# Kernel tuning notes

Measured on AMD Instinct MI355X. Metric: run time of the kernel, lower is better.

## Reference

```python
import jax, jax.numpy as jnp
import numpy as np

ALPHA, BETA, LAMB, GAMMA = 1.0, 1.0, 1e-4, 1.0
K_NN, TAU = 50, 0.1
EPS = 1e-8


def _sqdist(A, B):
    # ||a - b||^2, clamped at 0 like the torch code
    d2 = (A * A).sum(1)[:, None] + (B * B).sum(1)[None, :] - 2.0 * (A @ B.T)
    return jnp.maximum(d2, 0.0)


def _mmd(s, t):
    comb = jnp.concatenate([s, t], axis=0)
    sigma_sq = jax.lax.stop_gradient(jnp.median(_sqdist(comb, comb))) / 2.0
    sigma_sq = jnp.where(sigma_sq < 1e-6, jnp.float32(1.0), sigma_sq)
    g = 1.0 / (sigma_sq + EPS)
    kxx = jnp.exp(-g * _sqdist(s, s)).mean()
    kyy = jnp.exp(-g * _sqdist(t, t)).mean()
    kxy = jnp.exp(-g * _sqdist(s, t)).mean()
    return jnp.maximum(kxx + kyy - 2.0 * kxy, 0.0)


def setup_inputs() -> dict:
    key = jax.random.key(0)
    ks = jax.random.split(key, 8)
    B, d, N, Nq, K = 256, 128, 200000, 10000, K_NN
    q_batch = jax.random.normal(ks[0], (B, d), jnp.float32)
    X = jax.random.normal(ks[1], (N, d), jnp.float32)
    W = jax.random.normal(ks[2], (d, d), jnp.float32) * (1.0 / np.sqrt(d))
    b = jnp.zeros((d,), jnp.float32)
    pre_weights = jax.random.uniform(ks[3], (Nq, K), jnp.float32)
    pre_weights = pre_weights / pre_weights.sum(1, keepdims=True)
    pre_indices = jax.random.randint(ks[4], (Nq, K), 0, N)
    q_indices = jax.random.randint(ks[5], (B,), 0, Nq)
    idx = jax.random.randint(ks[6], (B,), 0, N)
    return {"q_batch": q_batch, "X": X, "W": W, "b": b,
            "pre_weights": pre_weights, "pre_indices": pre_indices,
            "q_indices": q_indices, "idx": idx}


def reference(q_batch, X, W, b, pre_weights, pre_indices, q_indices, idx):
    Tq = q_batch @ W.T + b                                   # model(q_batch), Linear(d, d)
    # ---- MMD between mapped queries and a random database batch ----
    loss_dist = _mmd(Tq, X[idx])
    # ---- exact KNN (faiss IndexFlatL2 equivalent) on detached embeddings ----
    d2_all = _sqdist(jax.lax.stop_gradient(Tq), X)           # [B, N]
    _, post_idx = jax.lax.top_k(-d2_all, K_NN)               # [B, K] nearest neighbors
    Xn = X[post_idx]                                         # [B, K, d]
    l2 = ((Tq[:, None, :] - Xn) ** 2).sum(-1)                # [B, K] (grad flows here)
    post_w = jax.nn.softmax(-l2 / TAU, axis=1)
    # ---- union-KL, vectorized over batch (exact torch.unique semantics) ----
    pre_i = pre_indices[q_indices]                           # [B, K]
    pre_w = pre_weights[q_indices]                           # [B, K]
    cat = jnp.concatenate([pre_i, post_idx], axis=1)         # [B, 2K]
    # multiplicity of each id within the concatenated list -> collapse duplicates
    mult = (cat[:, :, None] == cat[:, None, :]).sum(-1).astype(jnp.float32)  # [B, 2K]
    p_raw = jnp.einsum('bmk,bk->bm',
                       (cat[:, :, None] == pre_i[:, None, :]).astype(jnp.float32), pre_w)
    q_raw = jnp.einsum('bmk,bk->bm',
                       (cat[:, :, None] == post_idx[:, None, :]).astype(jnp.float32), post_w)
    p_c = jnp.maximum(p_raw, EPS)
    q_c = jnp.maximum(q_raw, EPS)
    p = p_c / (p_c / mult).sum(1, keepdims=True)             # normalize over union
    q = q_c / (q_c / mult).sum(1, keepdims=True)
    kl = ((p * (jnp.log(p) - jnp.log(q))) / mult).sum(1)     # KL(p || q) per sample
    loss_knn = kl.mean()
    # ---- L2 regularization of model params & anchor loss ----
    loss_reg = 0.5 * ((W ** 2).sum() + (b ** 2).sum())
    loss_anchor = ((Tq - q_batch) ** 2).sum(1).mean()
    total = ALPHA * loss_dist + BETA * loss_knn + LAMB * loss_reg + GAMMA * loss_anchor
    return jnp.stack([total, loss_dist, loss_knn, loss_anchor])
```

## Files before the change

### kernel.cpp

```cpp
#include <hip/hip_runtime.h>
#include <cstdint>

#define D 128
#define NPTS 200000
#define KNN 50
#define CAP 8192
#define NS 8192
#define SLACK 2.0f

#define OFF_ACC    0
#define OFF_SEL    256
#define OFF_CNT    1024
#define OFF_HIST0  17408
#define OFF_HIST12 148480
#define MEMSET_BYTES 214016
#define OFF_COMB   214016
#define OFF_D2     476160
#define OFF_XN     1524736
#define OFF_SAMP   2324736
#define OFF_THR    10713344
#define OFF_CANDI  10714368
#define OFF_KSG    19102976
#define OFF_TQSW   27491584
#define OFF_XBF    27557120

typedef __attribute__((ext_vector_type(8))) short bf16x8;
typedef __attribute__((ext_vector_type(4))) float f32x4;
typedef const __attribute__((address_space(1))) void* gas_p;
typedef __attribute__((address_space(3))) void* las_p;

__device__ __forceinline__ unsigned fkey(float f) {
    unsigned u = __float_as_uint(f);
    return u ^ ((unsigned)((int)u >> 31) | 0x80000000u);
}

__device__ __forceinline__ void stage8k(const unsigned short* __restrict__ g,
                                        unsigned short* l, int w, int lane)
{
    #pragma unroll
    for (int j = 0; j < 2; j++) {
        const unsigned short* gp = g + j * 2048 + w * 512 + lane * 8;
        unsigned short* lp = l + j * 2048 + w * 512;
        __builtin_amdgcn_global_load_lds((gas_p)gp, (las_p)lp, 16, 0, 0);
    }
}

__global__ void k_phase1(const float* __restrict__ q, const float* __restrict__ X,
                         const float* __restrict__ W, const float* __restrict__ bb,
                         const int* __restrict__ idx, float* __restrict__ comb,
                         unsigned short* __restrict__ tqsw, unsigned short* __restrict__ xbf,
                         float* __restrict__ xn, float* __restrict__ acc)
{
    const int blk = blockIdx.x, t = threadIdx.x;
    if (blk < 12500) {
        __shared__ float xr[16];
        const int lr = t & 15;
        if (t < 16) xr[t] = 0.f;
        __syncthreads();
        const float4* src = (const float4*)(X + ((long)(blk * 16 + lr)) * D + (t >> 4) * 8);
        float4 v0 = src[0], v1 = src[1];
        uint4 pk;
        pk.x = (__float_as_uint(v0.x) >> 16) | (__float_as_uint(v0.y) & 0xFFFF0000u);
        pk.y = (__float_as_uint(v0.z) >> 16) | (__float_as_uint(v0.w) & 0xFFFF0000u);
        pk.z = (__float_as_uint(v1.x) >> 16) | (__float_as_uint(v1.y) & 0xFFFF0000u);
        pk.w = (__float_as_uint(v1.z) >> 16) | (__float_as_uint(v1.w) & 0xFFFF0000u);
        *(uint4*)(xbf + (long)blk * 2048 + t * 8) = pk;
        float ssq = v0.x*v0.x + v0.y*v0.y + v0.z*v0.z + v0.w*v0.w
                  + v1.x*v1.x + v1.y*v1.y + v1.z*v1.z + v1.w*v1.w;
        atomicAdd(&xr[lr], ssq);
        __syncthreads();
        if (t < 16) xn[blk * 16 + t] = xr[t];
    } else if (blk < 12628) {
        __shared__ float rowv[2][D];
        __shared__ float red[2][D];
        const int half = t >> 7, tt = t & 127;
        const int row = (blk - 12500) * 2 + half;
        rowv[half][tt] = q[row * D + tt];
        __syncthreads();
        float s = 0.f;
        const float* wr = W + tt * D;
        #pragma unroll 4
        for (int k = 0; k < D; k++) s = fmaf(rowv[half][k], wr[k], s);
        s += bb[tt];
        comb[row * D + tt] = s;
        unsigned ub = __float_as_uint(s);
        unsigned short hv = (unsigned short)((ub + 0x7fffu + ((ub >> 16) & 1u)) >> 16);
        int ksb = tt >> 5, quad = (tt & 31) >> 3, jj = tt & 7;
        int lane = quad * 16 + (row & 15);
        tqsw[(row >> 4) * 2048 + ksb * 512 + lane * 8 + jj] = hv;
        float dd = s - rowv[half][tt];
        red[half][tt] = dd * dd;
        __syncthreads();
        for (int off = 64; off > 0; off >>= 1) { if (tt < off) red[half][tt] += red[half][tt + off]; __syncthreads(); }
        if (tt == 0) atomicAdd(&acc[0], red[half][0]);
    } else if (blk < 12756) {
        const int half = t >> 7, tt = t & 127;
        const int i = (blk - 12628) * 2 + half;
        comb[(256 + i) * D + tt] = X[(long)idx[i] * D + tt];
    } else {
        __shared__ float wred[4];
        const int base = (blk - 12756) * 4096;
        float s = 0.f;
        #pragma unroll 4
        for (int k = 0; k < 16; k++) { float v = W[base + k * 256 + t]; s = fmaf(v, v, s); }
        if (blk == 12756 && t < D) { float v = bb[t]; s = fmaf(v, v, s); }
        #pragma unroll
        for (int off = 32; off > 0; off >>= 1) s += __shfl_down(s, off);
        if ((t & 63) == 0) wred[t >> 6] = s;
        __syncthreads();
        if (t == 0) atomicAdd(&acc[7], wred[0] + wred[1] + wred[2] + wred[3]);
    }
}

__global__ void k_d2h(const float* __restrict__ comb, float* __restrict__ D2w,
                      unsigned* __restrict__ hist0)
{
    __shared__ float cj[64][D + 1];
    __shared__ float ci[4][D];
    __shared__ unsigned h[4096];
    const int ib = blockIdx.x, jb = blockIdx.y, t = threadIdx.x;
    const int w = t >> 6, l = t & 63;
    for (int m = t; m < 4096; m += 256) h[m] = 0;
    const int irow = ib * 4 + w;
    ci[w][l] = comb[irow * D + l];
    ci[w][l + 64] = comb[irow * D + l + 64];
    const float4* src = (const float4*)(comb + (jb * 64) * D);
    #pragma unroll
    for (int m = 0; m < 8; m++) {
        int u = m * 256 + t;
        int r = u >> 5, c = u & 31;
        float4 v = src[u];
        cj[r][c * 4 + 0] = v.x; cj[r][c * 4 + 1] = v.y; cj[r][c * 4 + 2] = v.z; cj[r][c * 4 + 3] = v.w;
    }
    __syncthreads();
    float s = 0.f;
    #pragma unroll 4
    for (int k = 0; k < D; k++) { float d = ci[w][k] - cj[l][k]; s = fmaf(d, d, s); }
    D2w[irow * 512 + jb * 64 + l] = s;
    atomicAdd(&h[__float_as_uint(s) >> 20], 1u);
    __syncthreads();
    const int sh = (ib + jb) & 7;
    for (int m = t; m < 4096; m += 256) { unsigned v = h[m]; if (v) atomicAdd(&hist0[m * 8 + sh], v); }
}

__global__ __launch_bounds__(256) void k_mf0(const unsigned short* __restrict__ tqsw,
    const unsigned short* __restrict__ xbf, const float* __restrict__ xn,
    float* __restrict__ samp, const unsigned* __restrict__ hist0, unsigned* __restrict__ sel)
{
    if (blockIdx.x == 256) {
        __shared__ unsigned part[256];
        const int t = threadIdx.x;
        unsigned s = 0;
        for (int m = 0; m < 16; m++) {
            int b = t * 16 + m;
            #pragma unroll
            for (int sh = 0; sh < 8; sh++) s += hist0[b * 8 + sh];
        }
        part[t] = s;
        __syncthreads();
        if (t == 0) {
            for (int tg = 0; tg < 2; tg++) {
                unsigned r = tg ? 131072u : 131071u;
                int c = 0;
                while (part[c] <= r) { r -= part[c]; c++; }
                int b = c * 16;
                while (true) {
                    unsigned bs = 0;
                    #pragma unroll
                    for (int sh = 0; sh < 8; sh++) bs += hist0[b * 8 + sh];
                    if (bs <= r) { r -= bs; b++; } else break;
                }
                sel[2 * tg] = (unsigned)b; sel[2 * tg + 1] = r;
            }
        }
        return;
    }
    __shared__ unsigned short sb[4096];
    const int t = threadIdx.x;
    const int w = t >> 6, lane = t & 63;
    const int lr = lane & 15, quad = lane >> 4;
    const int ck = blockIdx.x;
    stage8k(xbf + (long)ck * 4096, sb, w, lane);
    bf16x8 a[4][4];
    #pragma unroll
    for (int i = 0; i < 4; i++)
        #pragma unroll
        for (int ks = 0; ks < 4; ks++)
            a[i][ks] = *(const bf16x8*)(tqsw + (w * 4 + i) * 2048 + ks * 512 + lane * 8);
    __syncthreads();
    #pragma unroll
    for (int tt = 0; tt < 2; tt++) {
        const int r = (ck * 2 + tt) * 16 + lr;
        float xnv = xn[r];
        bf16x8 b[4];
        #pragma unroll
        for (int ks = 0; ks < 4; ks++)
            b[ks] = *(const bf16x8*)(sb + tt * 2048 + ks * 512 + lane * 8);
        f32x4 acc[4];
        #pragma unroll
        for (int i = 0; i < 4; i++) acc[i] = (f32x4){0.f, 0.f, 0.f, 0.f};
        #pragma unroll
        for (int ks = 0; ks < 4; ks++)
            #pragma unroll
            for (int i = 0; i < 4; i++)
                acc[i] = __builtin_amdgcn_mfma_f32_16x16x32_bf16(a[i][ks], b[ks], acc[i], 0, 0, 0);
        #pragma unroll
        for (int i = 0; i < 4; i++)
            #pragma unroll
            for (int reg = 0; reg < 4; reg++) {
                int qq = w * 64 + i * 16 + quad * 4 + reg;
                samp[qq * NS + r] = xnv - 2.f * acc[i][reg];
            }
    }
}

__global__ void k_h1thr(const float* __restrict__ D2w, unsigned* __restrict__ hist12,
                        const unsigned* __restrict__ sel, const float* __restrict__ samp,
                        float* __restrict__ thr)
{
    __shared__ unsigned buf[8192];
    __shared__ unsigned wred[4];
    const int t = threadIdx.x;
    if (blockIdx.x < 256) {
        for (int m = t; m < 8192; m += 256) buf[m] = 0;
        __syncthreads();
        unsigned p0 = sel[0], p1 = sel[2];
        const int e0 = blockIdx.x * 1024;
        for (int m = 0; m < 4; m++) {
            unsigned key = __float_as_uint(D2w[e0 + m * 256 + t]);
            if ((key >> 20) == p0) atomicAdd(&buf[(key >> 8) & 0xFFFu], 1u);
            if ((key >> 20) == p1) atomicAdd(&buf[4096 + ((key >> 8) & 0xFFFu)], 1u);
        }
        __syncthreads();
        for (int m = t; m < 8192; m += 256) { unsigned v = buf[m]; if (v) atomicAdd(&hist12[m], v); }
    } else {
        const int q = blockIdx.x - 256;
        for (int m = t; m < NS; m += 256) buf[m] = fkey(samp[q * NS + m]);
        __syncthreads();
        unsigned v = 0;
        for (int bit = 31; bit >= 0; bit--) {
            unsigned trial = v | (1u << bit);
            unsigned c = 0;
            for (int m = t; m < NS; m += 256) c += (buf[m] < trial) ? 1u : 0u;
            #pragma unroll
            for (int off = 32; off > 0; off >>= 1) c += __shfl_down(c, off);
            if ((t & 63) == 0) wred[t >> 6] = c;
            __syncthreads();
            unsigned total = wred[0] + wred[1] + wred[2] + wred[3];
            __syncthreads();
            if (total <= (unsigned)(KNN - 1)) v = trial;
        }
        if (t == 0) {
            unsigned orig = (v & 0x80000000u) ? (v ^ 0x80000000u) : ~v;
            thr[q] = __uint_as_float(orig) + SLACK;
        }
    }
}

__global__ void k_hist2s(const float* __restrict__ D2w, unsigned* __restrict__ hist12,
                         unsigned* __restrict__ sel)
{
    __shared__ unsigned h[8192];
    __shared__ unsigned part[256];
    __shared__ unsigned pfx[2];
    __shared__ unsigned rr[2];
    const int t = threadIdx.x;
    for (int tg = 0; tg < 2; tg++) {
        const unsigned* hh = hist12 + tg * 4096;
        unsigned s = 0;
        for (int m = 0; m < 16; m++) s += hh[t * 16 + m];
        part[t] = s;
        __syncthreads();
        if (t == 0) {
            unsigned r = sel[1 + 2 * tg];
            int c = 0;
            while (part[c] <= r) { r -= part[c]; c++; }
            int b = c * 16;
            while (hh[b] <= r) { r -= hh[b]; b++; }
            pfx[tg] = (sel[2 * tg] << 12) | (unsigned)b;
            rr[tg] = r;
        }
        __syncthreads();
    }
    if (blockIdx.x == 0 && t == 0) {
        sel[4] = pfx[0]; sel[5] = rr[0]; sel[6] = pfx[1]; sel[7] = rr[1];
    }
    for (int m = t; m < 8192; m += 256) h[m] = 0;
    __syncthreads();
    unsigned p0 = pfx[0], p1 = pfx[1];
    const int e0 = blockIdx.x * 1024;
    for (int m = 0; m < 4; m++) {
        unsigned key = __float_as_uint(D2w[e0 + m * 256 + t]);
        if ((key >> 8) == p0) atomicAdd(&h[key & 0xFFu], 1u);
        if ((key >> 8) == p1) atomicAdd(&h[4096 + (key & 0xFFu)], 1u);
    }
    __syncthreads();
    unsigned* gp = hist12 + 8192;
    for (int m = t; m < 8192; m += 256) { unsigned v = h[m]; if (v) atomicAdd(&gp[m], v); }
}

__global__ __launch_bounds__(256) void k_mf1(const unsigned short* __restrict__ tqsw,
    const unsigned short* __restrict__ xbf, const float* __restrict__ xn,
    const float* __restrict__ thr, int* __restrict__ cand_i, unsigned* __restrict__ cnt,
    const float* __restrict__ D2w, const unsigned* __restrict__ hist12,
    const unsigned* __restrict__ sel, float* __restrict__ acc)
{
    if (blockIdx.x >= 1024) {
        __shared__ unsigned h2[512];
        __shared__ float gsh;
        __shared__ float part[12];
        const int t = threadIdx.x, w = t >> 6;
        h2[t] = hist12[8192 + t];
        h2[256 + t] = hist12[8192 + 4096 + t];
        __syncthreads();
        if (t == 0) {
            unsigned key[2];
            for (int tg = 0; tg < 2; tg++) {
                unsigned r = sel[5 + 2 * tg];
                const unsigned* hh = h2 + tg * 256;
                int b = 0;
                while (hh[b] <= r) { r -= hh[b]; b++; }
                key[tg] = (sel[4 + 2 * tg] << 8) | (unsigned)b;
            }
            float med = 0.5f * (__uint_as_float(key[0]) + __uint_as_float(key[1]));
            float ssq = 0.5f * med;
            if (ssq < 1e-6f) ssq = 1.0f;
            gsh = 1.0f / (ssq + 1e-8f);
        }
        __syncthreads();
        const float g = gsh;
        float s[3] = {0.f, 0.f, 0.f};
        const int e0 = (blockIdx.x - 1024) * 1024;
        #pragma unroll
        for (int m = 0; m < 4; m++) {
            int e = e0 + m * 256 + t;
            int i = e >> 9, j = e & 511;
            float v = expf(-g * D2w[e]);
            int qd = (i < 256) ? ((j < 256) ? 0 : 2) : ((j < 256) ? 2 : 1);
            s[qd] += v;
        }
        #pragma unroll
        for (int c = 0; c < 3; c++) {
            float x = s[c];
            #pragma unroll
            for (int off = 32; off > 0; off >>= 1) x += __shfl_down(x, off);
            if ((t & 63) == 0) part[w * 3 + c] = x;
        }
        __syncthreads();
        if (t == 0)
            for (int c = 0; c < 3; c++)
                atomicAdd(&acc[2 + c], part[c] + part[3 + c] + part[6 + c] + part[9 + c]);
        return;
    }
    __shared__ unsigned short sb[2][4096];
    __shared__ unsigned lbuf[1024];
    __shared__ unsigned lcnt;
    const int t = threadIdx.x;
    const int w = t >> 6, lane = t & 63;
    const int lr = lane & 15, quad = lane >> 4;
    bf16x8 a[4][4];
    #pragma unroll
    for (int i = 0; i < 4; i++)
        #pragma unroll
        for (int ks = 0; ks < 4; ks++)
            a[i][ks] = *(const bf16x8*)(tqsw + (w * 4 + i) * 2048 + ks * 512 + lane * 8);
    float th_r[4][4];
    #pragma unroll
    for (int i = 0; i < 4; i++)
        #pragma unroll
        for (int reg = 0; reg < 4; reg++)
            th_r[i][reg] = thr[w * 64 + i * 16 + quad * 4 + reg];
    int ck = blockIdx.x;
    int cur = 0;
    if (t == 0) lcnt = 0;
    stage8k(xbf + (long)ck * 4096, sb[0], w, lane);
    __syncthreads();
    while (true) {
        const int ckn = ck + 1024;
        const bool has = ckn < 6250;
        if (has) stage8k(xbf + (long)ckn * 4096, sb[cur ^ 1], w, lane);
        #pragma unroll
        for (int tt = 0; tt < 2; tt++) {
            const int r = (ck * 2 + tt) * 16 + lr;
            float xnv = xn[r];
            bf16x8 b[4];
            #pragma unroll
            for (int ks = 0; ks < 4; ks++)
                b[ks] = *(const bf16x8*)(sb[cur] + tt * 2048 + ks * 512 + lane * 8);
            f32x4 acc4[4];
            #pragma unroll
            for (int i = 0; i < 4; i++) acc4[i] = (f32x4){0.f, 0.f, 0.f, 0.f};
            #pragma unroll
            for (int ks = 0; ks < 4; ks++)
                #pragma unroll
                for (int i = 0; i < 4; i++)
                    acc4[i] = __builtin_amdgcn_mfma_f32_16x16x32_bf16(a[i][ks], b[ks], acc4[i], 0, 0, 0);
            #pragma unroll
            for (int i = 0; i < 4; i++)
                #pragma unroll
                for (int reg = 0; reg < 4; reg++) {
                    float s = xnv - 2.f * acc4[i][reg];
                    if (s <= th_r[i][reg]) {
                        unsigned qq = (unsigned)(w * 64 + i * 16 + quad * 4 + reg);
                        unsigned p = atomicAdd(&lcnt, 1u);
                        if (p < 1024u) lbuf[p] = (qq << 18) | (unsigned)r;
                        else {
                            unsigned pos = atomicAdd(&cnt[qq * 16], 1u);
                            if (pos < CAP) cand_i[qq * CAP + pos] = r;
                        }
                    }
                }
        }
        __syncthreads();
        unsigned n = lcnt;
        if (!has || n >= 512u) {
            unsigned nf = (n < 1024u) ? n : 1024u;
            for (unsigned m = t; m < nf; m += 256) {
                unsigned e = lbuf[m];
                unsigned qq = e >> 18, r2 = e & 0x3FFFFu;
                unsigned pos = atomicAdd(&cnt[qq * 16], 1u);
                if (pos < CAP) cand_i[qq * CAP + pos] = (int)r2;
            }
            __syncthreads();
            if (t == 0) lcnt = 0;
            __syncthreads();
        }
        if (!has) break;
        ck = ckn; cur ^= 1;
    }
}

__global__ void k_rescore(const float* __restrict__ comb, const float* __restrict__ X,
                          const float* __restrict__ xn, const int* __restrict__ cand_i,
                          const unsigned* __restrict__ cnt, unsigned* __restrict__ ksg)
{
    __shared__ float qrow[D];
    const int q = blockIdx.x, sp = blockIdx.y, t = threadIdx.x;
    if (t < D) qrow[t] = comb[q * D + t];
    __syncthreads();
    unsigned nn = cnt[q * 16];
    const int n = (nn < (unsigned)CAP) ? (int)nn : CAP;
    const int g = t >> 3, j = t & 7;
    for (int m = sp * 32 + g; m < n; m += 512) {
        int r = cand_i[q * CAP + m];
        const float4* xr = (const float4*)(X + (long)r * D);
        float s = 0.f;
        #pragma unroll
        for (int p = 0; p < 4; p++) {
            float4 xv = xr[j * 4 + p];
            float4 qv = *(const float4*)&qrow[(j * 4 + p) * 4];
            s = fmaf(xv.x, qv.x, fmaf(xv.y, qv.y, fmaf(xv.z, qv.z, fmaf(xv.w, qv.w, s))));
        }
        s += __shfl_down(s, 4); s += __shfl_down(s, 2); s += __shfl_down(s, 1);
        if (j == 0) ksg[q * CAP + m] = fkey(xn[r] - 2.f * s);
    }
}

__global__ void k_post2(const float* __restrict__ comb, const float* __restrict__ X,
                        const int* __restrict__ cand_i, const unsigned* __restrict__ cnt,
                        const unsigned* __restrict__ ksg, const int* __restrict__ pri,
                        const float* __restrict__ prw, const int* __restrict__ qix,
                        float* __restrict__ acc)
{
    __shared__ unsigned ks[CAP];
    __shared__ float qrow[D];
    __shared__ unsigned wred[4];
    __shared__ unsigned wpos, eqn;
    __shared__ int eq[64];
    __shared__ int pidx[KNN];
    __shared__ float l2s[KNN];
    __shared__ float pw[KNN];
    __shared__ int ci[100];
    __shared__ float pwv[50], qwv[50];
    __shared__ float pterm[100], qterm[100], kterm[100];
    __shared__ float Sp, Sq;
    const int q = blockIdx.x, t = threadIdx.x;
    if (t < D) qrow[t] = comb[q * D + t];
    if (t == 0) { wpos = 0; eqn = 0; }
    unsigned nn = cnt[q * 16];
    const int n = (nn < (unsigned)CAP) ? (int)nn : CAP;
    for (int m = t; m < n; m += 256) ks[m] = ksg[q * CAP + m];
    __syncthreads();
    int kk = KNN - 1; if (kk > n - 1) kk = n - 1;
    unsigned v = 0;
    for (int bit = 31; bit >= 0; bit--) {
        unsigned trial = v | (1u << bit);
        unsigned c = 0;
        for (int m = t; m < n; m += 256) c += (ks[m] < trial) ? 1u : 0u;
        #pragma unroll
        for (int off = 32; off > 0; off >>= 1) c += __shfl_down(c, off);
        if ((t & 63) == 0) wred[t >> 6] = c;
        __syncthreads();
        unsigned total = wred[0] + wred[1] + wred[2] + wred[3];
        __syncthreads();
        if (total <= (unsigned)kk) v = trial;
    }
    for (int m = t; m < n; m += 256) {
        if (ks[m] < v) {
            unsigned p = atomicAdd(&wpos, 1u);
            pidx[p] = cand_i[q * CAP + m];
        } else if (ks[m] == v) {
            unsigned p = atomicAdd(&eqn, 1u);
            if (p < 64) eq[p] = cand_i[q * CAP + m];
        }
    }
    __syncthreads();
    if (t == 0) {
        int c1 = (int)wpos, need = KNN - c1;
        int ne = (eqn < 64u) ? (int)eqn : 64;
        for (int a = 0; a < ne; a++)
            for (int b2 = a + 1; b2 < ne; b2++)
                if (eq[b2] < eq[a]) { int tmp = eq[a]; eq[a] = eq[b2]; eq[b2] = tmp; }
        for (int a = 0; a < need && a < ne; a++) pidx[c1 + a] = eq[a];
    }
    __syncthreads();
    const int g = t >> 3, j = t & 7;
    for (int nb = g; nb < KNN; nb += 32) {
        long r = pidx[nb];
        const float4* xr = (const float4*)(X + r * D);
        float s = 0.f;
        #pragma unroll
        for (int p = 0; p < 4; p++) {
            float4 xv = xr[j * 4 + p];
            float4 qv = *(const float4*)&qrow[(j * 4 + p) * 4];
            float d0 = qv.x - xv.x, d1 = qv.y - xv.y, d2 = qv.z - xv.z, d3 = qv.w - xv.w;
            s += d0 * d0 + d1 * d1 + d2 * d2 + d3 * d3;
        }
        s += __shfl_down(s, 4); s += __shfl_down(s, 2); s += __shfl_down(s, 1);
        if (j == 0) l2s[nb] = s;
    }
    int qi = qix[q];
    if (t >= 128 && t < 178) { int k = t - 128; ci[k] = pri[qi * 50 + k]; pwv[k] = prw[qi * 50 + k]; }
    __syncthreads();
    if (t < 64) {
        float logit = (t < KNN) ? (-l2s[t] * 10.0f) : -3.4e38f;
        float m = logit;
        #pragma unroll
        for (int off = 32; off > 0; off >>= 1) m = fmaxf(m, __shfl_down(m, off));
        m = __shfl(m, 0);
        float e = (t < KNN) ? expf(logit - m) : 0.f;
        float ss = e;
        #pragma unroll
        for (int off = 32; off > 0; off >>= 1) ss += __shfl_down(ss, off);
        ss = __shfl(ss, 0);
        if (t < KNN) pw[t] = e / ss;
    }
    __syncthreads();
    if (t < 50) { ci[50 + t] = pidx[t]; qwv[t] = pw[t]; }
    __syncthreads();
    float pc = 0.f, qc = 0.f, mult = 0.f;
    if (t < 100) {
        int c = ci[t];
        float pr = 0.f, qr = 0.f;
        for (int k = 0; k < 50; k++) {
            bool m1 = (c == ci[k]); bool m2 = (c == ci[50 + k]);
            mult += (m1 ? 1.f : 0.f) + (m2 ? 1.f : 0.f);
            pr += m1 ? pwv[k] : 0.f;
            qr += m2 ? qwv[k] : 0.f;
        }
        pc = fmaxf(pr, 1e-8f); qc = fmaxf(qr, 1e-8f);
        pterm[t] = pc / mult; qterm[t] = qc / mult;
    }
    __syncthreads();
    if (t == 0) { float a = 0.f, b2 = 0.f; for (int m = 0; m < 100; m++) { a += pterm[m]; b2 += qterm[m]; } Sp = a; Sq = b2; }
    __syncthreads();
    if (t < 100) {
        float p = pc / Sp, qq2 = qc / Sq;
        kterm[t] = (p * (logf(p) - logf(qq2))) / mult;
    }
    __syncthreads();
    if (t == 0) { float s = 0.f; for (int m = 0; m < 100; m++) s += kterm[m]; atomicAdd(&acc[1], s); }
}

__global__ void k_final(const float* __restrict__ acc, float* __restrict__ out)
{
    if (threadIdx.x == 0) {
        float reg = 0.5f * acc[7];
        float kxx = acc[2] / 65536.f, kyy = acc[3] / 65536.f, kxy = acc[4] / 131072.f;
        float ld = fmaxf(kxx + kyy - 2.f * kxy, 0.f);
        float lknn = acc[1] / 256.f;
        float lanc = acc[0] / 256.f;
        out[0] = ld + lknn + 1e-4f * reg + lanc;
        out[1] = ld; out[2] = lknn; out[3] = lanc;
    }
}

extern "C" void kernel_launch(void* const* d_in, const int* in_sizes, int n_in,
                              void* d_out, int out_size, void* d_ws, size_t ws_size,
                              hipStream_t stream)
{
    (void)in_sizes; (void)n_in; (void)out_size; (void)ws_size;
    const float* q   = (const float*)d_in[0];
    const float* X   = (const float*)d_in[1];
    const float* W   = (const float*)d_in[2];
    const float* bb  = (const float*)d_in[3];
    const float* prw = (const float*)d_in[4];
    const int*   pri = (const int*)d_in[5];
    const int*   qix = (const int*)d_in[6];
    const int*   idx = (const int*)d_in[7];
    float* out = (float*)d_out;
    char* ws = (char*)d_ws;
    float*    acc   = (float*)(ws + OFF_ACC);
    unsigned* sel   = (unsigned*)(ws + OFF_SEL);
    unsigned* cnt   = (unsigned*)(ws + OFF_CNT);
    unsigned* hist0 = (unsigned*)(ws + OFF_HIST0);
    unsigned* hist12= (unsigned*)(ws + OFF_HIST12);
    float*    comb  = (float*)(ws + OFF_COMB);
    float*    D2w   = (float*)(ws + OFF_D2);
    float*    xn    = (float*)(ws + OFF_XN);
    float*    samp  = (float*)(ws + OFF_SAMP);
    float*    thr   = (float*)(ws + OFF_THR);
    int*      cix   = (int*)(ws + OFF_CANDI);
    unsigned* ksg   = (unsigned*)(ws + OFF_KSG);
    unsigned short* tqsw = (unsigned short*)(ws + OFF_TQSW);
    unsigned short* xbf  = (unsigned short*)(ws + OFF_XBF);

    hipMemsetAsync(ws, 0, MEMSET_BYTES, stream);
    hipLaunchKernelGGL(k_phase1,  dim3(12760),   dim3(256), 0, stream, q, X, W, bb, idx, comb, tqsw, xbf, xn, acc);
    hipLaunchKernelGGL(k_d2h,     dim3(128, 8),  dim3(256), 0, stream, comb, D2w, hist0);
    hipLaunchKernelGGL(k_mf0,     dim3(257),     dim3(256), 0, stream, tqsw, xbf, xn, samp, hist0, sel);
    hipLaunchKernelGGL(k_h1thr,   dim3(512),     dim3(256), 0, stream, D2w, hist12, sel, samp, thr);
    hipLaunchKernelGGL(k_hist2s,  dim3(256),     dim3(256), 0, stream, D2w, hist12, sel);
    hipLaunchKernelGGL(k_mf1,     dim3(1280),    dim3(256), 0, stream, tqsw, xbf, xn, thr, cix, cnt, D2w, hist12, sel, acc);
    hipLaunchKernelGGL(k_rescore, dim3(256, 16), dim3(256), 0, stream, comb, X, xn, cix, cnt, ksg);
    hipLaunchKernelGGL(k_post2,   dim3(256),     dim3(256), 0, stream, comb, X, cix, cnt, ksg, pri, prw, qix, acc);
    hipLaunchKernelGGL(k_final,   dim3(1),       dim3(64),  0, stream, acc, out);
}
```

Before: 419.6 us.

## Buffer KNN candidates per block, then scatter to per-query lists in a separate kernel

The MFMA filter kernel no longer does global atomics on per-query counters for every candidate. Each block appends packed (query,row) entries to its own private global buffer with a plain contiguous write. A new scatter kernel builds a per-query histogram in shared memory over 8 blocks' buffers, reserves ranges with one global atomic per query, and writes the candidate indices. This removes contended global atomics from the hot loop, at the cost of an extra launch, an extra pass over the entries, and silent truncation when a block's buffer exceeds 2048 entries.

```diff
diff --git a/kernel.cpp b/kernel.cpp
--- a/kernel.cpp
+++ b/kernel.cpp
@@ -7,6 +7,7 @@
 #define CAP 8192
 #define NS 8192
 #define SLACK 2.0f
+#define EB 2048
 
 #define OFF_ACC    0
 #define OFF_SEL    256
@@ -18,9 +19,11 @@
 #define OFF_D2     476160
 #define OFF_XN     1524736
 #define OFF_SAMP   2324736
+#define OFF_EBUF   2324736
 #define OFF_THR    10713344
 #define OFF_CANDI  10714368
 #define OFF_KSG    19102976
+#define OFF_BCNT   19102976
 #define OFF_TQSW   27491584
 #define OFF_XBF    27557120
 
@@ -301,7 +304,7 @@
 
 __global__ __launch_bounds__(256) void k_mf1(const unsigned short* __restrict__ tqsw,
     const unsigned short* __restrict__ xbf, const float* __restrict__ xn,
-    const float* __restrict__ thr, int* __restrict__ cand_i, unsigned* __restrict__ cnt,
+    const float* __restrict__ thr, unsigned* __restrict__ ebuf, unsigned* __restrict__ bcnt,
     const float* __restrict__ D2w, const unsigned* __restrict__ hist12,
     const unsigned* __restrict__ sel, float* __restrict__ acc)
 {
@@ -355,9 +358,11 @@
     __shared__ unsigned short sb[2][4096];
     __shared__ unsigned lbuf[1024];
     __shared__ unsigned lcnt;
+    __shared__ unsigned gbase;
     const int t = threadIdx.x;
     const int w = t >> 6, lane = t & 63;
     const int lr = lane & 15, quad = lane >> 4;
+    unsigned* eb = ebuf + (unsigned)blockIdx.x * EB;
     bf16x8 a[4][4];
     #pragma unroll
     for (int i = 0; i < 4; i++)
@@ -372,7 +377,7 @@
             th_r[i][reg] = thr[w * 64 + i * 16 + quad * 4 + reg];
     int ck = blockIdx.x;
     int cur = 0;
-    if (t == 0) lcnt = 0;
+    if (t == 0) { lcnt = 0; gbase = 0; }
     stage8k(xbf + (long)ck * 4096, sb[0], w, lane);
     __syncthreads();
     while (true) {
@@ -405,8 +410,8 @@
                         unsigned p = atomicAdd(&lcnt, 1u);
                         if (p < 1024u) lbuf[p] = (qq << 18) | (unsigned)r;
                         else {
-                            unsigned pos = atomicAdd(&cnt[qq * 16], 1u);
-                            if (pos < CAP) cand_i[qq * CAP + pos] = r;
+                            unsigned d = gbase + p;
+                            if (d < EB) eb[d] = (qq << 18) | (unsigned)r;
                         }
                     }
                 }
@@ -415,18 +420,52 @@
         unsigned n = lcnt;
         if (!has || n >= 512u) {
             unsigned nf = (n < 1024u) ? n : 1024u;
+            unsigned gb = gbase;
             for (unsigned m = t; m < nf; m += 256) {
-                unsigned e = lbuf[m];
-                unsigned qq = e >> 18, r2 = e & 0x3FFFFu;
-                unsigned pos = atomicAdd(&cnt[qq * 16], 1u);
-                if (pos < CAP) cand_i[qq * CAP + pos] = (int)r2;
+                unsigned d = gb + m;
+                if (d < EB) eb[d] = lbuf[m];
             }
             __syncthreads();
-            if (t == 0) lcnt = 0;
+            if (t == 0) { gbase = gb + n; lcnt = 0; }
             __syncthreads();
         }
         if (!has) break;
         ck = ckn; cur ^= 1;
+    }
+    if (t == 0) bcnt[blockIdx.x] = (gbase < EB) ? gbase : EB;
+}
+
+__global__ __launch_bounds__(256) void k_scat(const unsigned* __restrict__ ebuf,
+    const unsigned* __restrict__ bcnt, int* __restrict__ cand_i, unsigned* __restrict__ cnt)
+{
+    __shared__ unsigned hist[256];
+    __shared__ unsigned startp[256];
+    const int t = threadIdx.x;
+    const int b0 = blockIdx.x * 8;
+    hist[t] = 0;
+    __syncthreads();
+    for (int b = b0; b < b0 + 8; b++) {
+        unsigned n = bcnt[b];
+        const unsigned* e = ebuf + (unsigned)b * EB;
+        for (unsigned m = t; m < n; m += 256)
+            atomicAdd(&hist[e[m] >> 18], 1u);
+    }
+    __syncthreads();
+    unsigned c = hist[t];
+    if (c) {
+        unsigned base = atomicAdd(&cnt[t * 16], c);
+        startp[t] = ((unsigned)t << 13) + base;
+    }
+    __syncthreads();
+    for (int b = b0; b < b0 + 8; b++) {
+        unsigned n = bcnt[b];
+        const unsigned* e = ebuf + (unsigned)b * EB;
+        for (unsigned m = t; m < n; m += 256) {
+            unsigned ent = e[m];
+            unsigned qq = ent >> 18;
+            unsigned pos = atomicAdd(&startp[qq], 1u);
+            if (pos < ((qq + 1u) << 13)) cand_i[pos] = (int)(ent & 0x3FFFFu);
+        }
     }
 }
 
@@ -612,6 +651,8 @@
     float*    thr   = (float*)(ws + OFF_THR);
     int*      cix   = (int*)(ws + OFF_CANDI);
     unsigned* ksg   = (unsigned*)(ws + OFF_KSG);
+    unsigned* ebuf  = (unsigned*)(ws + OFF_EBUF);
+    unsigned* bcnt  = (unsigned*)(ws + OFF_BCNT);
     unsigned short* tqsw = (unsigned short*)(ws + OFF_TQSW);
     unsigned short* xbf  = (unsigned short*)(ws + OFF_XBF);
 
@@ -621,7 +662,8 @@
     hipLaunchKernelGGL(k_mf0,     dim3(257),     dim3(256), 0, stream, tqsw, xbf, xn, samp, hist0, sel);
     hipLaunchKernelGGL(k_h1thr,   dim3(512),     dim3(256), 0, stream, D2w, hist12, sel, samp, thr);
     hipLaunchKernelGGL(k_hist2s,  dim3(256),     dim3(256), 0, stream, D2w, hist12, sel);
-    hipLaunchKernelGGL(k_mf1,     dim3(1280),    dim3(256), 0, stream, tqsw, xbf, xn, thr, cix, cnt, D2w, hist12, sel, acc);
+    hipLaunchKernelGGL(k_mf1,     dim3(1280),    dim3(256), 0, stream, tqsw, xbf, xn, thr, ebuf, bcnt, D2w, hist12, sel, acc);
+    hipLaunchKernelGGL(k_scat,    dim3(128),     dim3(256), 0, stream, ebuf, bcnt, cix, cnt);
     hipLaunchKernelGGL(k_rescore, dim3(256, 16), dim3(256), 0, stream, comb, X, xn, cix, cnt, ksg);
     hipLaunchKernelGGL(k_post2,   dim3(256),     dim3(256), 0, stream, comb, X, cix, cnt, ksg, pri, prw, qix, acc);
     hipLaunchKernelGGL(k_final,   dim3(1),       dim3(64),  0, stream, acc, out);
```

New measurement: 397.3 us. 5.3% less time.
